# Kernel tuning notes

Hardware: AMD Instinct MI355X
Metric: run time of the kernel (lower is better)

## Reference

```python
import jax, jax.numpy as jnp
import numpy as np

D_IN = 2048
D_OUT = 2048
BOUND = 1.0


def setup_inputs() -> dict:
    key = jax.random.key(0)
    kx, kw = jax.random.split(key)
    x = jax.random.normal(kx, (4, 2048, D_IN), dtype=jnp.float32)
    W_raw = 0.02 * jax.random.normal(kw, (D_OUT, D_IN), dtype=jnp.float32)
    return {"x": x, "W_raw": W_raw}


def reference(x, W_raw):
    # sigma = ||W||_2 (largest singular value), exact via SVD
    sigma = jnp.linalg.svd(W_raw, full_matrices=False, compute_uv=False)[0]
    scale = jnp.maximum(sigma / BOUND, 1.0)  # clamp(sigma/bound, min=1)
    Wn = W_raw / scale                        # [d_out, d_in]
    return jnp.einsum('bsi,oi->bso', x, Wn)   # x @ Wn.T
```

## Files before the change

### kernel.cpp

```cpp
#include <hip/hip_runtime.h>
#include <stdint.h>

typedef short bf16x8 __attribute__((ext_vector_type(8)));
typedef float f32x4 __attribute__((ext_vector_type(4)));

__device__ __forceinline__ unsigned short f2bf(float f) {
  union { float f; unsigned int u; } v; v.f = f;
  unsigned int u = v.u;
  return (unsigned short)((u + 0x7FFFu + ((u >> 16) & 1u)) >> 16);
}
__device__ __forceinline__ float bf2f(unsigned short u) {
  union { unsigned int u; float f; } v; v.u = ((unsigned int)u) << 16;
  return v.f;
}
__device__ __forceinline__ void async16(const void* g, void* l) {
  __builtin_amdgcn_global_load_lds(
      (const __attribute__((address_space(1))) unsigned int*)g,
      (__attribute__((address_space(3))) unsigned int*)l, 16, 0, 0);
}
__device__ __forceinline__ void cast8(const float4 a, const float4 b,
                                      unsigned short* dst) {
  union { bf16x8 v; unsigned short s[8]; } o;
  o.s[0] = f2bf(a.x); o.s[1] = f2bf(a.y); o.s[2] = f2bf(a.z); o.s[3] = f2bf(a.w);
  o.s[4] = f2bf(b.x); o.s[5] = f2bf(b.y); o.s[6] = f2bf(b.z); o.s[7] = f2bf(b.w);
  *(bf16x8*)dst = o.v;
}
__device__ __forceinline__ float dot8(bf16x8 a, float4 v0, float4 v1) {
  return bf2f((unsigned short)a[0]) * v0.x + bf2f((unsigned short)a[1]) * v0.y +
         bf2f((unsigned short)a[2]) * v0.z + bf2f((unsigned short)a[3]) * v0.w +
         bf2f((unsigned short)a[4]) * v1.x + bf2f((unsigned short)a[5]) * v1.y +
         bf2f((unsigned short)a[6]) * v1.z + bf2f((unsigned short)a[7]) * v1.w;
}

__global__ __launch_bounds__(256) void cast_f32_bf16(
    const float* __restrict__ in, unsigned short* __restrict__ out, int n8) {
  int i = blockIdx.x * 256 + threadIdx.x;
  if (i >= n8) return;
  const float4* p = (const float4*)in;
  cast8(p[2 * (size_t)i], p[2 * (size_t)i + 1], out + 8 * (size_t)i);
}

__device__ __forceinline__ void stage16k(const unsigned short* __restrict__ g0,
                                         int ldK, unsigned short* lds, int tid) {
#pragma unroll
  for (int q = 0; q < 2; ++q) {
    int idx = q * 512 + tid;
    int r = idx >> 3;
    int jj = (idx & 7) ^ (r & 7);
    async16(g0 + (size_t)r * ldK + jj * 8,
            lds + ((size_t)(q * 512 + (tid & ~63))) * 8);
  }
}

template <int OMODE>
__global__ __launch_bounds__(512, 2) void gemm256(
    const unsigned short* __restrict__ A, const unsigned short* __restrict__ B,
    void* __restrict__ Cv, int M, int N, int lda, int K,
    int nTn, int mT, const float* __restrict__ scale_ptr) {
  __shared__ __align__(16) unsigned short AsBuf[3][256 * 64];
  __shared__ __align__(16) unsigned short BsBuf[2][256 * 64];
  const int tid = threadIdx.x;
  const int w = tid >> 6, lane = tid & 63;
  int bid = blockIdx.x;
  const int mb = bid % mT; bid /= mT;
  const int nb = bid % nTn; const int ks = bid / nTn;
  const int m0 = mb * 256, n0 = nb * 256;
  const int wr = w >> 2, wc = w & 3;
  const int R = K >> 7;

  const unsigned short* Ab = A + (size_t)m0 * lda + (size_t)ks * K;
  const unsigned short* Bb = B + (size_t)n0 * lda + (size_t)ks * K;

  unsigned short *a0 = AsBuf[0], *a1 = AsBuf[1], *a2 = AsBuf[2];
  unsigned short *b0 = BsBuf[0], *b1 = BsBuf[1];

  stage16k(Ab,                          lda, a0,            tid);
  stage16k(Ab + (size_t)128 * lda,      lda, a0 + 128 * 64, tid);
  stage16k(Bb,                          lda, b0,            tid);
  stage16k(Bb + (size_t)128 * lda,      lda, b0 + 128 * 64, tid);
  stage16k(Ab + 64,                     lda, a1,            tid);
  stage16k(Ab + 64 + (size_t)128 * lda, lda, a1 + 128 * 64, tid);
  stage16k(Bb + 64,                     lda, b1,            tid);
  stage16k(Bb + 64 + (size_t)128 * lda, lda, b1 + 128 * 64, tid);
  asm volatile("s_waitcnt vmcnt(8)" ::: "memory");
  __builtin_amdgcn_s_barrier();
  asm volatile("" ::: "memory");

  const int fr = lane & 15;
  const int bc0 = ((lane >> 4) << 4) ^ ((fr & 7) << 4);
  const int bc1 = bc0 ^ 64;

  f32x4 acc[8][4] = {};

  for (int r = 0; r < R; ++r) {
    const bool st = (r + 1 < R);
    bf16x8 bg[4][2];
#pragma unroll
    for (int ph = 0; ph < 8; ++ph) {
      const int d = ph >> 2, q = ph & 3;
      const char* cA = (const char*)(d == 0 ? a0 : a1);
      const char* cB = (const char*)(d == 0 ? b0 : b1);
      if (q == 0) {
#pragma unroll
        for (int nf = 0; nf < 4; ++nf) {
          int rb = (wc * 64 + nf * 16 + fr) * 128;
          bg[nf][0] = *(const bf16x8*)(cB + rb + bc0);
          bg[nf][1] = *(const bf16x8*)(cB + rb + bc1);
        }
      }
      bf16x8 af[2][2];
#pragma unroll
      for (int m2 = 0; m2 < 2; ++m2) {
        int rb = (wr * 128 + q * 32 + m2 * 16 + fr) * 128;
        af[m2][0] = *(const bf16x8*)(cA + rb + bc0);
        af[m2][1] = *(const bf16x8*)(cA + rb + bc1);
      }
      if (st) switch (ph) {
        case 0: stage16k(Ab + (size_t)(2 * r + 2) * 64, lda, a2, tid); break;
        case 1: stage16k(Ab + (size_t)(2 * r + 2) * 64 + (size_t)128 * lda, lda,
                         a2 + 128 * 64, tid); break;
        case 2: stage16k(Bb + (size_t)(2 * r + 2) * 64, lda, b0, tid); break;
        case 3: stage16k(Bb + (size_t)(2 * r + 2) * 64 + (size_t)128 * lda, lda,
                         b0 + 128 * 64, tid); break;
        case 4: stage16k(Ab + (size_t)(2 * r + 3) * 64, lda, a0, tid); break;
        case 5: stage16k(Ab + (size_t)(2 * r + 3) * 64 + (size_t)128 * lda, lda,
                         a0 + 128 * 64, tid); break;
        case 6: stage16k(Bb + (size_t)(2 * r + 3) * 64, lda, b1, tid); break;
        case 7: stage16k(Bb + (size_t)(2 * r + 3) * 64 + (size_t)128 * lda, lda,
                         b1 + 128 * 64, tid); break;
      }
      asm volatile("" ::: "memory");
      __builtin_amdgcn_s_barrier();
      asm volatile("" ::: "memory");
      __builtin_amdgcn_s_setprio(1);
#pragma unroll
      for (int m2 = 0; m2 < 2; ++m2)
#pragma unroll
        for (int nf = 0; nf < 4; ++nf)
#pragma unroll
          for (int kh = 0; kh < 2; ++kh)
            acc[q * 2 + m2][nf] = __builtin_amdgcn_mfma_f32_16x16x32_bf16(
                af[m2][kh], bg[nf][kh], acc[q * 2 + m2][nf], 0, 0, 0);
      __builtin_amdgcn_s_setprio(0);
      asm volatile("" ::: "memory");
      if (ph == 3) {
        if (st) asm volatile("s_waitcnt vmcnt(8)" ::: "memory");
        else    asm volatile("s_waitcnt vmcnt(0)" ::: "memory");
      } else if (ph == 7) {
        if (st) asm volatile("s_waitcnt vmcnt(8)" ::: "memory");
      }
      __builtin_amdgcn_s_barrier();
      asm volatile("" ::: "memory");
    }
    unsigned short* t = a2; a2 = a1; a1 = a0; a0 = t;
  }

  float sc = 1.0f;
  if (OMODE == 1) sc = *scale_ptr;
  size_t base = (OMODE == 2) ? (size_t)ks * ((size_t)M * N) : 0;
  const int rr0 = m0 + wr * 128 + ((lane >> 4) << 2);
  const int cc0 = n0 + wc * 64 + fr;
#pragma unroll
  for (int mf = 0; mf < 8; ++mf)
#pragma unroll
    for (int nf = 0; nf < 4; ++nf)
#pragma unroll
      for (int tt = 0; tt < 4; ++tt) {
        size_t idx = base + (size_t)(rr0 + mf * 16 + tt) * N + (cc0 + nf * 16);
        if (OMODE == 2) ((unsigned short*)Cv)[idx] = f2bf(acc[mf][nf][tt]);
        else            ((float*)Cv)[idx] = acc[mf][nf][tt] * sc;
      }
}

__global__ __launch_bounds__(512) void gemv_first(
    const unsigned short* __restrict__ P, unsigned short* __restrict__ Aout,
    size_t plane, float* __restrict__ tout) {
  __shared__ __align__(16) float vs[2048];
  __shared__ float wred[8];
  const int tid = threadIdx.x;
  const int wv = tid >> 6, lane = tid & 63;
  const int row = blockIdx.x * 8 + wv;

  float t0[4]; float ss = 0.f;
#pragma unroll
  for (int j = 0; j < 4; ++j) {
    int idx = tid * 4 + j;
    unsigned int h = (unsigned int)idx * 2654435761u;
    h ^= h >> 16; h *= 2246822519u; h ^= h >> 13;
    t0[j] = (float)(h & 0xFFFFu) * (1.0f / 65536.0f) - 0.5f;
    ss += t0[j] * t0[j];
  }
#pragma unroll
  for (int o = 32; o > 0; o >>= 1) ss += __shfl_xor(ss, o);
  if (lane == 0) wred[wv] = ss;
  __syncthreads();
  float n2 = 0.f;
#pragma unroll
  for (int j = 0; j < 8; ++j) n2 += wred[j];
  float inv = 1.0f / sqrtf(n2);
#pragma unroll
  for (int j = 0; j < 4; ++j) vs[tid * 4 + j] = t0[j] * inv;
  __syncthreads();

  const size_t rbase = (size_t)row * 2048;
  float s = 0.f;
#pragma unroll
  for (int c4 = 0; c4 < 4; ++c4) {
    int c = lane + c4 * 64;
    float a8[8] = {0.f, 0.f, 0.f, 0.f, 0.f, 0.f, 0.f, 0.f};
#pragma unroll
    for (int p = 0; p < 4; ++p) {
      bf16x8 v = *(const bf16x8*)(P + p * plane + rbase + (size_t)c * 8);
#pragma unroll
      for (int j = 0; j < 8; ++j) a8[j] += bf2f((unsigned short)v[j]);
    }
    union { bf16x8 v; unsigned short u[8]; } o;
#pragma unroll
    for (int j = 0; j < 8; ++j) o.u[j] = f2bf(a8[j]);
    *(bf16x8*)(Aout + rbase + (size_t)c * 8) = o.v;
    float4 v0 = ((const float4*)vs)[2 * c], v1 = ((const float4*)vs)[2 * c + 1];
    s += a8[0] * v0.x + a8[1] * v0.y + a8[2] * v0.z + a8[3] * v0.w +
         a8[4] * v1.x + a8[5] * v1.y + a8[6] * v1.z + a8[7] * v1.w;
  }
#pragma unroll
  for (int o = 32; o > 0; o >>= 1) s += __shfl_xor(s, o);
  if (lane == 0) tout[row] = s;
}

template <int MODE>
__global__ __launch_bounds__(512) void gemv_step(
    const unsigned short* __restrict__ Am, const float* __restrict__ tin,
    float* __restrict__ tout, float* __restrict__ ch, float* __restrict__ aux,
    const float* __restrict__ xsrc, unsigned short* __restrict__ xdst,
    int u0, int u1) {
  __shared__ __align__(16) float vs[2048];
  __shared__ float wred[8];
  const int tid = threadIdx.x;
  const int wv = tid >> 6, lane = tid & 63;
  const int row = blockIdx.x * 8 + wv;

  const bf16x8* Ar = (const bf16x8*)(Am + (size_t)row * 2048);
  bf16x8 ar0 = Ar[lane], ar1 = Ar[lane + 64];
  bf16x8 ar2 = Ar[lane + 128], ar3 = Ar[lane + 192];
  const int cu0 = u0 + blockIdx.x * 512 + tid;
  const int cu1 = cu0 + 131072;
  const bool cd0 = cu0 < u1, cd1 = cu1 < u1;
  float4 ca0, cb0, ca1, cb1;
  const float4* xp = (const float4*)xsrc;
  if (cd0) { ca0 = xp[2 * (size_t)cu0]; cb0 = xp[2 * (size_t)cu0 + 1]; }
  if (cd1) { ca1 = xp[2 * (size_t)cu1]; cb1 = xp[2 * (size_t)cu1 + 1]; }

  float ymv = 0.f, chv = 0.f;
  if (MODE == 3) { ymv = aux[row]; chv = ch[0]; }

  float4 x0 = ((const float4*)tin)[tid];
  float sin_ = 1.0f;
  if (MODE != 3) {
    float ss = x0.x * x0.x + x0.y * x0.y + x0.z * x0.z + x0.w * x0.w;
#pragma unroll
    for (int o = 32; o > 0; o >>= 1) ss += __shfl_xor(ss, o);
    if (lane == 0) wred[wv] = ss;
    __syncthreads();
    float n2 = 0.f;
#pragma unroll
    for (int j = 0; j < 8; ++j) n2 += wred[j];
    float nrm = sqrtf(n2);
    if (MODE == 2) {
      chv = nrm;
      if (blockIdx.x == 0 && tid == 0) ch[0] = nrm;
    }
    sin_ = 1.0f / nrm;
  }
  float4 y = {x0.x * sin_, x0.y * sin_, x0.z * sin_, x0.w * sin_};
  ((float4*)vs)[tid] = y;
  __syncthreads();

  const float4* vp = (const float4*)vs;
  float s = dot8(ar0, vp[2 * lane], vp[2 * lane + 1]);
  s += dot8(ar1, vp[2 * (lane + 64)], vp[2 * (lane + 64) + 1]);
  s += dot8(ar2, vp[2 * (lane + 128)], vp[2 * (lane + 128) + 1]);
  s += dot8(ar3, vp[2 * (lane + 192)], vp[2 * (lane + 192) + 1]);
#pragma unroll
  for (int o = 32; o > 0; o >>= 1) s += __shfl_xor(s, o);
  if (lane == 0) {
    float r;
    if (MODE == 0)      r = s;
    else if (MODE == 2) r = (2.0f / chv) * s - vs[row];
    else                r = (4.0f / chv) * s - 2.0f * vs[row] - ymv;
    tout[row] = r;
    if (MODE == 2) aux[row] = vs[row];
  }
  if (cd0) cast8(ca0, cb0, xdst + 8 * (size_t)cu0);
  if (cd1) cast8(ca1, cb1, xdst + 8 * (size_t)cu1);
}

__global__ __launch_bounds__(256) void finalize_sigma(
    const float* __restrict__ tk, float* __restrict__ inv_scale) {
  __shared__ float wred[4];
  const int tid = threadIdx.x;
  float4 x0 = ((const float4*)tk)[2 * tid];
  float4 x1 = ((const float4*)tk)[2 * tid + 1];
  float ss = x0.x * x0.x + x0.y * x0.y + x0.z * x0.z + x0.w * x0.w +
             x1.x * x1.x + x1.y * x1.y + x1.z * x1.z + x1.w * x1.w;
#pragma unroll
  for (int o = 32; o > 0; o >>= 1) ss += __shfl_xor(ss, o);
  if ((tid & 63) == 0) wred[tid >> 6] = ss;
  __syncthreads();
  if (tid == 0) {
    float lam = sqrtf(wred[0] + wred[1] + wred[2] + wred[3]);
    float sigma = sqrtf(lam);
    float scl = fmaxf(sigma, 1.0f);
    inv_scale[0] = 1.0f / scl;
  }
}

extern "C" void kernel_launch(void* const* d_in, const int* in_sizes, int n_in,
                              void* d_out, int out_size, void* d_ws, size_t ws_size,
                              hipStream_t stream) {
  (void)in_sizes; (void)n_in; (void)out_size; (void)ws_size;
  const float* x = (const float*)d_in[0];
  const float* W = (const float*)d_in[1];
  float* out = (float*)d_out;
  char* ws = (char*)d_ws;
  const int K = 2048, N = 2048, M = 4 * 2048;
  const size_t PLANE = (size_t)2048 * 2048;

  unsigned short* xb = (unsigned short*)(ws);
  unsigned short* Wb = (unsigned short*)(ws + ((size_t)32 << 20));
  unsigned short* P1 = (unsigned short*)(ws + ((size_t)40 << 20));
  unsigned short* Am = P1;
  float* tv = (float*)(ws + ((size_t)72 << 20));
  float* tb0 = tv, *tb1 = tv + 2048, *tb2 = tv + 4096;
  float* inv_scale = tv + 6144;
  float* cshift = tv + 6146;
  float* tb[3] = {tb0, tb1, tb2};

  cast_f32_bf16<<<(N * K / 8 + 255) / 256, 256, 0, stream>>>(W, Wb, N * K / 8);

  gemm256<2><<<256, 512, 0, stream>>>(Wb, Wb, P1, 2048, 2048, 2048, 512, 8, 8, nullptr);
  gemv_first<<<256, 512, 0, stream>>>(P1, Am, PLANE, tb1);

  const int XU = M * K / 8;
  const int NL = 17;
  const int CH = (XU + NL - 1) / NL;
  int li = 0;
#define SLICE x, xb, (li) * CH, min((li + 1) * CH, XU)); ++li
  gemv_step<0><<<256, 512, 0, stream>>>(Am, tb1, tb0, cshift, tb2, SLICE;
  gemv_step<0><<<256, 512, 0, stream>>>(Am, tb0, tb1, cshift, tb2, SLICE;
  gemv_step<2><<<256, 512, 0, stream>>>(Am, tb1, tb2, cshift, tb0, SLICE;
  int cy = 2, cm = 0;
  for (int k = 0; k < 13; ++k) {
    int co = 3 - cy - cm;
    gemv_step<3><<<256, 512, 0, stream>>>(Am, tb[cy], tb[co], cshift, tb[cm], SLICE;
    cm = cy; cy = co;
  }
  int co = 3 - cy - cm;
  gemv_step<0><<<256, 512, 0, stream>>>(Am, tb[cy], tb[co], cshift, tb[cm], SLICE;
#undef SLICE
  finalize_sigma<<<1, 256, 0, stream>>>(tb[co], inv_scale);

  gemm256<1><<<256, 512, 0, stream>>>(xb, Wb, out, M, N, K, K, 8, 32, inv_scale);
}
```

Before: 170.1 us.

## Skew MFMA k-halves across phases and fold sigma finalize into GEMM epilogue

The GEMM inner loop now splits each phase's two k-halves so the second half of the previous phase's A fragments is consumed one phase later. The B fragment loads are likewise split across two phases. This spreads LDS reads and lets MFMA issue overlap with the fragment loads, at the cost of extra live registers and an epilogue MFMA drain. It also removes the single-block finalize_sigma launch: every GEMM wave recomputes the norm of the 2048-element vector itself in the epilogue, trading one launch for redundant reads per wave.

```diff
diff --git a/kernel.cpp b/kernel.cpp
--- a/kernel.cpp
+++ b/kernel.cpp
@@ -91,13 +91,15 @@
   const int bc1 = bc0 ^ 64;
 
   f32x4 acc[8][4] = {};
+  bf16x8 bg[4][2] = {};
+  bf16x8 afp[2] = {};
 
   for (int r = 0; r < R; ++r) {
     const bool st = (r + 1 < R);
-    bf16x8 bg[4][2];
 #pragma unroll
     for (int ph = 0; ph < 8; ++ph) {
       const int d = ph >> 2, q = ph & 3;
+      const int pq = ((ph + 7) & 7) & 3;
       const char* cA = (const char*)(d == 0 ? a0 : a1);
       const char* cB = (const char*)(d == 0 ? b0 : b1);
       if (q == 0) {
@@ -105,6 +107,12 @@
         for (int nf = 0; nf < 4; ++nf) {
           int rb = (wc * 64 + nf * 16 + fr) * 128;
           bg[nf][0] = *(const bf16x8*)(cB + rb + bc0);
+        }
+      }
+      if (q == 1) {
+#pragma unroll
+        for (int nf = 0; nf < 4; ++nf) {
+          int rb = (wc * 64 + nf * 16 + fr) * 128;
           bg[nf][1] = *(const bf16x8*)(cB + rb + bc1);
         }
       }
@@ -137,11 +145,19 @@
       for (int m2 = 0; m2 < 2; ++m2)
 #pragma unroll
         for (int nf = 0; nf < 4; ++nf)
-#pragma unroll
-          for (int kh = 0; kh < 2; ++kh)
-            acc[q * 2 + m2][nf] = __builtin_amdgcn_mfma_f32_16x16x32_bf16(
-                af[m2][kh], bg[nf][kh], acc[q * 2 + m2][nf], 0, 0, 0);
+          acc[q * 2 + m2][nf] = __builtin_amdgcn_mfma_f32_16x16x32_bf16(
+              af[m2][0], bg[nf][0], acc[q * 2 + m2][nf], 0, 0, 0);
+      if (ph != 0 || r > 0) {
+#pragma unroll
+        for (int m2 = 0; m2 < 2; ++m2)
+#pragma unroll
+          for (int nf = 0; nf < 4; ++nf)
+            acc[pq * 2 + m2][nf] = __builtin_amdgcn_mfma_f32_16x16x32_bf16(
+                afp[m2], bg[nf][1], acc[pq * 2 + m2][nf], 0, 0, 0);
+      }
       __builtin_amdgcn_s_setprio(0);
+      afp[0] = af[0][1];
+      afp[1] = af[1][1];
       asm volatile("" ::: "memory");
       if (ph == 3) {
         if (st) asm volatile("s_waitcnt vmcnt(8)" ::: "memory");
@@ -154,9 +170,27 @@
     }
     unsigned short* t = a2; a2 = a1; a1 = a0; a0 = t;
   }
+#pragma unroll
+  for (int m2 = 0; m2 < 2; ++m2)
+#pragma unroll
+    for (int nf = 0; nf < 4; ++nf)
+      acc[3 * 2 + m2][nf] = __builtin_amdgcn_mfma_f32_16x16x32_bf16(
+          afp[m2], bg[nf][1], acc[3 * 2 + m2][nf], 0, 0, 0);
 
   float sc = 1.0f;
-  if (OMODE == 1) sc = *scale_ptr;
+  if (OMODE == 1) {
+    const float4* tvp = (const float4*)scale_ptr;
+    float ss = 0.f;
+#pragma unroll
+    for (int j = 0; j < 8; ++j) {
+      float4 v = tvp[lane * 8 + j];
+      ss += v.x * v.x + v.y * v.y + v.z * v.z + v.w * v.w;
+    }
+#pragma unroll
+    for (int o = 32; o > 0; o >>= 1) ss += __shfl_xor(ss, o);
+    float sigma = sqrtf(sqrtf(ss));
+    sc = 1.0f / fmaxf(sigma, 1.0f);
+  }
   size_t base = (OMODE == 2) ? (size_t)ks * ((size_t)M * N) : 0;
   const int rr0 = m0 + wr * 128 + ((lane >> 4) << 2);
   const int cc0 = n0 + wc * 64 + fr;
@@ -294,26 +328,6 @@
   if (cd1) cast8(ca1, cb1, xdst + 8 * (size_t)cu1);
 }
 
-__global__ __launch_bounds__(256) void finalize_sigma(
-    const float* __restrict__ tk, float* __restrict__ inv_scale) {
-  __shared__ float wred[4];
-  const int tid = threadIdx.x;
-  float4 x0 = ((const float4*)tk)[2 * tid];
-  float4 x1 = ((const float4*)tk)[2 * tid + 1];
-  float ss = x0.x * x0.x + x0.y * x0.y + x0.z * x0.z + x0.w * x0.w +
-             x1.x * x1.x + x1.y * x1.y + x1.z * x1.z + x1.w * x1.w;
-#pragma unroll
-  for (int o = 32; o > 0; o >>= 1) ss += __shfl_xor(ss, o);
-  if ((tid & 63) == 0) wred[tid >> 6] = ss;
-  __syncthreads();
-  if (tid == 0) {
-    float lam = sqrtf(wred[0] + wred[1] + wred[2] + wred[3]);
-    float sigma = sqrtf(lam);
-    float scl = fmaxf(sigma, 1.0f);
-    inv_scale[0] = 1.0f / scl;
-  }
-}
-
 extern "C" void kernel_launch(void* const* d_in, const int* in_sizes, int n_in,
                               void* d_out, int out_size, void* d_ws, size_t ws_size,
                               hipStream_t stream) {
@@ -331,7 +345,6 @@
   unsigned short* Am = P1;
   float* tv = (float*)(ws + ((size_t)72 << 20));
   float* tb0 = tv, *tb1 = tv + 2048, *tb2 = tv + 4096;
-  float* inv_scale = tv + 6144;
   float* cshift = tv + 6146;
   float* tb[3] = {tb0, tb1, tb2};
 
@@ -357,7 +370,6 @@
   int co = 3 - cy - cm;
   gemv_step<0><<<256, 512, 0, stream>>>(Am, tb[cy], tb[co], cshift, tb[cm], SLICE;
 #undef SLICE
-  finalize_sigma<<<1, 256, 0, stream>>>(tb[co], inv_scale);
-
-  gemm256<1><<<256, 512, 0, stream>>>(xb, Wb, out, M, N, K, K, 8, 32, inv_scale);
-}
+
+  gemm256<1><<<256, 512, 0, stream>>>(xb, Wb, out, M, N, K, K, 8, 32, tb[co]);
+}
```

Result: no change. 168.8 us (-0.7%).
